# Performance work log

Measured on AMD Instinct MI355X. Metric: run time of the kernel, lower is better.

Reference implementation:

```python
import jax, jax.numpy as jnp
import numpy as np

EPS = 1e-5  # torch InstanceNorm2d default eps


def conv1x1(x, w, b):
    # x: [B,C,H,W], w: [O,C], b: [O]
    return jnp.einsum('bchw,oc->bohw', x, w) + b[None, :, None, None]


def conv3x3(x, w, b):
    y = jax.lax.conv_general_dilated(x, w, (1, 1), 'SAME',
                                     dimension_numbers=('NCHW', 'OIHW', 'NCHW'))
    return y + b[None, :, None, None]


def inorm(x):
    # InstanceNorm2d, affine=False, biased variance
    m = jnp.mean(x, axis=(2, 3), keepdims=True)
    v = jnp.var(x, axis=(2, 3), keepdims=True)
    return (x - m) * jax.lax.rsqrt(v + EPS)


def self_attn(x, wq, bq, wk, bk, wv, bv, gamma):
    B, C, H, W = x.shape
    N = H * W
    q = conv1x1(x, wq, bq).reshape(B, -1, N)   # [B,C/8,N]
    k = conv1x1(x, wk, bk).reshape(B, -1, N)   # [B,C/8,N]
    A = jax.nn.softmax(jnp.einsum('bdn,bdm->bnm', q, k), axis=-1)  # [B,N,N]
    v = conv1x1(x, wv, bv).reshape(B, C, N)    # [B,C,N]
    out = jnp.einsum('bcm,bnm->bcn', v, A).reshape(B, C, H, W)
    return gamma * out + x


def setup_inputs() -> dict:
    key = jax.random.key(0)
    B, C, H, W = 2, 256, 64, 64
    C8 = C // 8
    ks = iter(jax.random.split(key, 40))

    def n(shape, scale=0.05):
        return jax.random.normal(next(ks), shape, dtype=jnp.float32) * scale

    inp = {
        'x': jax.random.normal(next(ks), (B, C, H, W), dtype=jnp.float32),
        'y': jax.random.normal(next(ks), (B, C, H, W), dtype=jnp.float32),
    }
    for p in ('sa1', 'sa2', 'top'):
        inp[p + '_wq'] = n((C8, C)); inp[p + '_bq'] = n((C8,))
        inp[p + '_wk'] = n((C8, C)); inp[p + '_bk'] = n((C8,))
        inp[p + '_wv'] = n((C, C));  inp[p + '_bv'] = n((C,))
        inp[p + '_gamma'] = n((1,), 0.1)
    inp['conv1_w'] = n((C, C, 3, 3)); inp['conv1_b'] = n((C,))
    inp['conv2_w'] = n((C, C, 3, 3)); inp['conv2_b'] = n((C,))
    return inp


def reference(x, y,
              sa1_wq, sa1_bq, sa1_wk, sa1_bk, sa1_wv, sa1_bv, sa1_gamma,
              sa2_wq, sa2_bq, sa2_wk, sa2_bk, sa2_wv, sa2_bv, sa2_gamma,
              top_wq, top_bq, top_wk, top_bk, top_wv, top_bv, top_gamma,
              conv1_w, conv1_b, conv2_w, conv2_b):
    out_1 = inorm(self_attn(x, sa1_wq, sa1_bq, sa1_wk, sa1_bk, sa1_wv, sa1_bv, sa1_gamma))
    out_2 = inorm(out_1 + conv3x3(out_1, conv1_w, conv1_b))
    out_3 = inorm(self_attn(y, sa2_wq, sa2_bq, sa2_wk, sa2_bk, sa2_wv, sa2_bv, sa2_gamma))

    B, C, H, W = out_2.shape
    N = H * W
    q = conv1x1(out_2, top_wq, top_bq).reshape(B, -1, N)
    k = conv1x1(out_2, top_wk, top_bk).reshape(B, -1, N)
    A = jax.nn.softmax(jnp.einsum('bdn,bdm->bnm', q, k), axis=-1)
    v = conv1x1(out_3, top_wv, top_bv).reshape(B, C, N)
    out = jnp.einsum('bcm,bnm->bcn', v, A).reshape(B, C, H, W)
    out = top_gamma * out + y
    out = inorm(out)
    out = inorm(out + out_3)
    out_4 = conv3x3(out, conv2_w, conv2_b)
    out = inorm(out + out_4)
    return out
```

## Files before the change

kernel.cpp:

```cpp
#include <hip/hip_runtime.h>
#include <hip/hip_bf16.h>

typedef __hip_bfloat16 bf16;
typedef __attribute__((ext_vector_type(8))) short s8v;
typedef __attribute__((ext_vector_type(4))) short s4v;
typedef __attribute__((ext_vector_type(4))) float f4v;

#define NPIX 4096
#define CDIM 256
#define MN_ELEMS (1 << 20)
#define QKVSTR (320L * NPIX)
#define QKTSTR (64L * NPIX)

#if __has_builtin(__builtin_amdgcn_exp2f)
#define EXP2F(x) __builtin_amdgcn_exp2f(x)
#else
#define EXP2F(x) exp2f(x)
#endif

typedef __attribute__((address_space(1))) const unsigned int g_u32;
typedef __attribute__((address_space(3))) unsigned int l_u32;
__device__ __forceinline__ void glds16(const void* g, void* l) {
  __builtin_amdgcn_global_load_lds((g_u32*)g, (l_u32*)l, 16, 0, 0);
}

__device__ inline s8v ld8(const bf16* p) { return *(const s8v*)p; }
__device__ inline s8v ld8(const float* p) {
  float4 f0 = *(const float4*)p;
  float4 f1 = *(const float4*)(p + 4);
  s8v r; bf16* e = (bf16*)&r;
  e[0] = __float2bfloat16(f0.x); e[1] = __float2bfloat16(f0.y);
  e[2] = __float2bfloat16(f0.z); e[3] = __float2bfloat16(f0.w);
  e[4] = __float2bfloat16(f1.x); e[5] = __float2bfloat16(f1.y);
  e[6] = __float2bfloat16(f1.z); e[7] = __float2bfloat16(f1.w);
  return r;
}

template<int NT>
__global__ __launch_bounds__(256) void fattn_k(
    const bf16* __restrict__ qkt, const bf16* __restrict__ Vg,
    bf16* __restrict__ out)
{
  constexpr int SN = NT / 32;
  __shared__ bf16 k_s[128 * 32];
  __shared__ bf16 v_s[4 * 128 * 32];
  __shared__ bf16 p_s[4 * NT * 32];
  float* sums = (float*)k_s;

  const int tid = threadIdx.x;
  const int z = blockIdx.z;
  const int w = tid >> 6, lane = tid & 63;
  const int l15 = lane & 15, oct = lane >> 4;
  const int wr = w >> 1, wc = w & 1;
  const int n0 = blockIdx.x * NT, c0 = blockIdx.y * 128;
  const bf16* qk = qkt + (long)z * QKTSTR;
  const bf16* Vz = Vg + (long)z * QKVSTR;
  const int srow = lane >> 2, scol = (lane & 3) * 8;

  #pragma unroll
  for (int g = 0; g < NT / 64; ++g)
    glds16(qk + (long)(n0 + g * 64 + (w << 4) + srow) * 64 + scol,
           p_s + g * 2048 + w * 512);
  glds16(qk + (long)((w << 4) + srow) * 64 + 32 + scol, k_s + w * 512);
  glds16(qk + (long)(64 + (w << 4) + srow) * 64 + 32 + scol, k_s + 2048 + w * 512);
  #pragma unroll
  for (int g = 0; g < 8; ++g) {
    const int kk = g & 3, rg = g >> 2;
    glds16(Vz + (long)(c0 + rg * 64 + (w << 4) + srow) * 4096 + kk * 32 + scol,
           v_s + kk * 4096 + rg * 2048 + w * 512);
  }
  __syncthreads();

  s8v qf[SN];
  #pragma unroll
  for (int st = 0; st < SN; ++st)
    qf[st] = *(const s8v*)(p_s + (wr * (NT / 2) + st * 16 + l15) * 32 + oct * 8);
  __syncthreads();

  f4v acc[4][SN];
  #pragma unroll
  for (int i = 0; i < 4; ++i)
    #pragma unroll
    for (int j = 0; j < SN; ++j) acc[i][j] = (f4v){0.f, 0.f, 0.f, 0.f};
  float rs[SN];
  #pragma unroll
  for (int st = 0; st < SN; ++st) rs[st] = 0.f;

  for (int i = 0; i < 32; ++i) {
    s8v kf[4];
    #pragma unroll
    for (int nt = 0; nt < 4; ++nt)
      kf[nt] = *(const s8v*)(k_s + (wc * 64 + nt * 16 + l15) * 32 + oct * 8);
    #pragma unroll
    for (int st = 0; st < SN; ++st) {
      const int n = wr * (NT / 2) + st * 16 + l15;
      const int sw = ((n >> 1) & 3) << 4;
      f4v sa[4];
      __builtin_amdgcn_s_setprio(1);
      #pragma unroll
      for (int nt = 0; nt < 4; ++nt) {
        f4v zz = (f4v){0.f, 0.f, 0.f, 0.f};
        sa[nt] = __builtin_amdgcn_mfma_f32_16x16x32_bf16(kf[nt], qf[st], zz, 0, 0, 0);
      }
      __builtin_amdgcn_s_setprio(0);
      #pragma unroll
      for (int nt = 0; nt < 4; ++nt) {
        const int kk = wc * 2 + (nt >> 1);
        int byte = kk * (NT * 64) + n * 64 + (nt & 1) * 32 + oct * 8;
        byte ^= sw;
        s4v pk; bf16* pe = (bf16*)&pk;
        float rsum = 0.f;
        #pragma unroll
        for (int r = 0; r < 4; ++r) {
          float e = EXP2F(sa[nt][r]);
          rsum += e;
          pe[r] = __float2bfloat16(e);
        }
        rs[st] += rsum;
        *(s4v*)((char*)p_s + byte) = pk;
      }
    }
    __syncthreads();
    #pragma unroll
    for (int kk = 0; kk < 4; ++kk) {
      s8v vf[4], pf[SN];
      #pragma unroll
      for (int st = 0; st < 4; ++st)
        vf[st] = *(const s8v*)(v_s + kk * 4096 + (wr * 64 + st * 16 + l15) * 32 + oct * 8);
      #pragma unroll
      for (int nt = 0; nt < SN; ++nt) {
        const int n = wc * (NT / 2) + nt * 16 + l15;
        int byte = kk * (NT * 64) + n * 64 + oct * 16;
        byte ^= ((n >> 1) & 3) << 4;
        pf[nt] = *(const s8v*)((const char*)p_s + byte);
      }
      __builtin_amdgcn_s_setprio(1);
      #pragma unroll
      for (int st = 0; st < 4; ++st)
        #pragma unroll
        for (int nt = 0; nt < SN; ++nt)
          acc[st][nt] = __builtin_amdgcn_mfma_f32_16x16x32_bf16(vf[st], pf[nt], acc[st][nt], 0, 0, 0);
      __builtin_amdgcn_s_setprio(0);
    }
    __syncthreads();
    if (i < 31) {
      const int m1 = (i + 1) * 128;
      glds16(qk + (long)(m1 + (w << 4) + srow) * 64 + 32 + scol, k_s + w * 512);
      glds16(qk + (long)(m1 + 64 + (w << 4) + srow) * 64 + 32 + scol, k_s + 2048 + w * 512);
      #pragma unroll
      for (int g = 0; g < 8; ++g) {
        const int kk = g & 3, rg = g >> 2;
        glds16(Vz + (long)(c0 + rg * 64 + (w << 4) + srow) * 4096 + m1 + kk * 32 + scol,
               v_s + kk * 4096 + rg * 2048 + w * 512);
      }
      __syncthreads();
    }
  }

  #pragma unroll
  for (int st = 0; st < SN; ++st) {
    rs[st] += __shfl_xor(rs[st], 16);
    rs[st] += __shfl_xor(rs[st], 32);
  }
  if (lane < 16) {
    #pragma unroll
    for (int st = 0; st < SN; ++st)
      sums[wc * NT + wr * (NT / 2) + st * 16 + l15] = rs[st];
  }
  __syncthreads();

  float rinv[SN];
  #pragma unroll
  for (int nt = 0; nt < SN; ++nt) {
    const int n = wc * (NT / 2) + nt * 16 + l15;
    rinv[nt] = 1.f / (sums[n] + sums[NT + n]);
  }
  bf16* op = out + (long)z * ((long)CDIM * NPIX);
  #pragma unroll
  for (int st = 0; st < 4; ++st) {
    const int gc = c0 + wr * 64 + st * 16 + oct * 4;
    #pragma unroll
    for (int nt = 0; nt < SN; ++nt) {
      const int gn = n0 + wc * (NT / 2) + nt * 16 + l15;
      #pragma unroll
      for (int r = 0; r < 4; ++r)
        op[(long)(gc + r) * NPIX + gn] = __float2bfloat16(acc[st][nt][r] * rinv[nt]);
    }
  }
}

__global__ __launch_bounds__(512) void conv_k(
    const bf16* __restrict__ x, const bf16* __restrict__ wcvt,
    const float* __restrict__ bias, bf16* __restrict__ out)
{
  __shared__ bf16 lds[3 * 66 * 66];
  const int tid = threadIdx.x;
  const int h = blockIdx.x;
  const int o0 = blockIdx.y * 128;
  x   += (long)blockIdx.z * CDIM * NPIX;
  out += (long)blockIdx.z * CDIM * NPIX;

  const int w = tid >> 6, lane = tid & 63;
  const int l15 = lane & 15, oct = lane >> 4;

  if (tid < 192) {
    int row = tid >> 6, c = tid & 63;
    lds[(row * 66 + 0) * 66 + c] = __float2bfloat16(0.f);
    lds[(row * 66 + 65) * 66 + c] = __float2bfloat16(0.f);
  }

  f4v acc[4];
  #pragma unroll
  for (int nf = 0; nf < 4; ++nf) acc[nf] = (f4v){0.f, 0.f, 0.f, 0.f};

  const int w2 = tid & 31, chi = tid >> 5;
  const long arow = (long)(o0 + w * 16 + l15) * 2304;

  for (int cg = 0; cg < 4; ++cg) {
    __syncthreads();
    #pragma unroll
    for (int it = 0; it < 12; ++it) {
      int row = it >> 2, cgi = it & 3;
      int c = cgi * 16 + chi;
      int hh = h + row - 1;
      unsigned int pix = 0;
      if ((unsigned)hh < 64u)
        pix = *(const unsigned int*)(x + (long)(cg * 64 + c) * 4096 + hh * 64 + w2 * 2);
      const bf16* pp = (const bf16*)&pix;
      lds[(row * 66 + (w2 * 2 + 1)) * 66 + c] = pp[0];
      lds[(row * 66 + (w2 * 2 + 2)) * 66 + c] = pp[1];
    }
    __syncthreads();

    #pragma unroll
    for (int j = 0; j < 9; ++j) {
      const int dy = j / 3, dx = j % 3;
      #pragma unroll
      for (int kc = 0; kc < 2; ++kc) {
        s8v af = *(const s8v*)(wcvt + arow + j * 256 + cg * 64 + kc * 32 + oct * 8);
        s8v bfv[4];
        #pragma unroll
        for (int nf = 0; nf < 4; ++nf)
          bfv[nf] = *(const s8v*)&lds[(dy * 66 + (nf * 16 + l15 + dx)) * 66 + kc * 32 + oct * 8];
        #pragma unroll
        for (int nf = 0; nf < 4; ++nf)
          acc[nf] = __builtin_amdgcn_mfma_f32_16x16x32_bf16(af, bfv[nf], acc[nf], 0, 0, 0);
      }
    }
  }

  #pragma unroll
  for (int nf = 0; nf < 4; ++nf) {
    const int gn = h * 64 + nf * 16 + l15;
    const int go = o0 + w * 16 + oct * 4;
    #pragma unroll
    for (int r = 0; r < 4; ++r)
      out[(long)(go + r) * NPIX + gn] = __float2bfloat16(acc[nf][r] + bias[go + r]);
  }
}

template<int QKT, typename TBe>
__global__ __launch_bounds__(256) void proj_k(
    const float* __restrict__ A, const float* __restrict__ A2,
    const TBe* __restrict__ B1, const TBe* __restrict__ B2,
    const float* __restrict__ bias, const float* __restrict__ bias2,
    bf16* __restrict__ Cm, bf16* __restrict__ qkt,
    int M, int N, int K, long bbat, long cbat, int nchunk)
{
  __shared__ bf16 a_s[64][40];
  __shared__ bf16 b_s[64][40];
  const int tid = threadIdx.x;
  const int z = blockIdx.z, stage = z >> 1, bat = z & 1;
  const float* Au = stage ? A2 : A;
  const float* biasu = stage ? bias2 : bias;
  const TBe* Bm = (stage ? B2 : B1) + bat * bbat;
  Cm += z * cbat;
  if (QKT) qkt += z * QKTSTR;
  const int m0 = blockIdx.y * 64, n0 = blockIdx.x * 64;
  const int w = tid >> 6, lane = tid & 63;
  const int l15 = lane & 15, oct = lane >> 4;

  f4v acc[4];
  #pragma unroll
  for (int i = 0; i < 4; ++i) acc[i] = (f4v){0.f, 0.f, 0.f, 0.f};

  const int a_i0 = tid >> 2, a_i1 = (tid & 3) * 8;
  const int b_i0 = tid >> 3, b_i1 = (tid & 7) * 8;

  s8v pa, pb;
  auto ldA = [&](int kc, s8v& d) {
    if (m0 + a_i0 < M) d = ld8(Au + (long)(m0 + a_i0) * K + kc * 32 + a_i1);
    else d = (s8v){0,0,0,0,0,0,0,0};
  };
  auto ldB = [&](int kc, s8v& d) {
    d = ld8(Bm + (long)(kc * 32 + b_i0) * N + n0 + b_i1);
  };

  ldA(0, pa); ldB(0, pb);
  for (int kc = 0; kc < nchunk; ++kc) {
    *(s8v*)&a_s[a_i0][a_i1] = pa;
    {
      const bf16* e = (const bf16*)&pb;
      #pragma unroll
      for (int j = 0; j < 8; ++j) b_s[b_i1 + j][b_i0] = e[j];
    }
    __syncthreads();
    if (kc + 1 < nchunk) { ldA(kc + 1, pa); ldB(kc + 1, pb); }
    s8v af = *(const s8v*)&a_s[w * 16 + l15][oct * 8];
    #pragma unroll
    for (int nt = 0; nt < 4; ++nt) {
      s8v bfr = *(const s8v*)&b_s[nt * 16 + l15][oct * 8];
      acc[nt] = __builtin_amdgcn_mfma_f32_16x16x32_bf16(af, bfr, acc[nt], 0, 0, 0);
    }
    __syncthreads();
  }
  const int gm_base = m0 + w * 16 + oct * 4;
  #pragma unroll
  for (int nt = 0; nt < 4; ++nt) {
    const int gn = n0 + nt * 16 + l15;
    #pragma unroll
    for (int r = 0; r < 4; ++r) {
      int gm = gm_base + r;
      if (gm < M) {
        float vv = acc[nt][r] + biasu[gm];
        if (QKT && gm < 64) {
          float vv2 = (gm < 32) ? vv * 1.44269504f : vv;
          qkt[(long)gn * 64 + gm] = __float2bfloat16(vv2);
        } else {
          Cm[(long)gm * N + gn] = __float2bfloat16(vv);
        }
      }
    }
  }
}

__global__ __launch_bounds__(256) void cat_k(
    const float* __restrict__ wq, const float* __restrict__ bq,
    const float* __restrict__ wk, const float* __restrict__ bk,
    const float* __restrict__ wv, const float* __restrict__ bv,
    float* __restrict__ wcat, float* __restrict__ bcat, int M)
{
  int idx = blockIdx.x * 256 + threadIdx.x;
  int total = M << 8;
  if (idx < total) {
    int r = idx >> 8, c = idx & 255;
    float v;
    if (r < 32) v = wq[r * 256 + c];
    else if (r < 64) v = wk[(r - 32) * 256 + c];
    else v = wv[(r - 64) * 256 + c];
    wcat[idx] = v;
  } else if (idx < total + M) {
    int r = idx - total;
    bcat[r] = (r < 32) ? bq[r] : (r < 64) ? bk[r - 32] : bv[r - 64];
  }
}

__global__ __launch_bounds__(256) void cvtw2_k(
    const float* __restrict__ w1, const float* __restrict__ w2,
    bf16* __restrict__ o1, bf16* __restrict__ o2)
{
  const float* in = blockIdx.y ? w2 : w1;
  bf16* out = blockIdx.y ? o2 : o1;
  int idx = blockIdx.x * 256 + threadIdx.x;
  int o = idx / 2304, r = idx % 2304;
  int j = r >> 8, c = r & 255;
  out[idx] = __float2bfloat16(in[(o * 256 + c) * 9 + j]);
}

__device__ inline void ld16(const bf16* p, float* v) {
  s8v r0 = *(const s8v*)p, r1 = *(const s8v*)(p + 8);
  const bf16* e0 = (const bf16*)&r0; const bf16* e1 = (const bf16*)&r1;
  #pragma unroll
  for (int j = 0; j < 8; ++j) { v[j] = __bfloat162float(e0[j]); v[8 + j] = __bfloat162float(e1[j]); }
}
__device__ inline void ld16(const float* p, float* v) {
  #pragma unroll
  for (int q = 0; q < 4; ++q) {
    float4 f = *(const float4*)(p + q * 4);
    v[q * 4 + 0] = f.x; v[q * 4 + 1] = f.y; v[q * 4 + 2] = f.z; v[q * 4 + 3] = f.w;
  }
}
__device__ inline void st16(bf16* p, const float* v) {
  s8v o0, o1v; bf16* f0 = (bf16*)&o0; bf16* f1 = (bf16*)&o1v;
  #pragma unroll
  for (int j = 0; j < 8; ++j) { f0[j] = __float2bfloat16(v[j]); f1[j] = __float2bfloat16(v[8 + j]); }
  *(s8v*)p = o0; *(s8v*)(p + 8) = o1v;
}
__device__ inline void st16(float* p, const float* v) {
  #pragma unroll
  for (int q = 0; q < 4; ++q) {
    float4 f; f.x = v[q * 4 + 0]; f.y = v[q * 4 + 1]; f.z = v[q * 4 + 2]; f.w = v[q * 4 + 3];
    *(float4*)(p + q * 4) = f;
  }
}

template<typename TAe, typename TBe, typename TOe, int G>
__global__ __launch_bounds__(256) void inorm_k(
    const TAe* __restrict__ a, const TBe* __restrict__ b,
    const float* __restrict__ g, TOe* __restrict__ out)
{
  __shared__ float red[8];
  const int tid = threadIdx.x;
  const long base = (long)blockIdx.x * NPIX + tid * 16;
  float gv = G ? *g : 1.f;
  float va[16], vbv[16], v[16];
  ld16(a + base, va);
  ld16(b + base, vbv);
  #pragma unroll
  for (int j = 0; j < 16; ++j) v[j] = gv * va[j] + vbv[j];
  float sum = 0.f, sq = 0.f;
  #pragma unroll
  for (int j = 0; j < 16; ++j) { sum += v[j]; sq += v[j] * v[j]; }
  #pragma unroll
  for (int s = 32; s; s >>= 1) { sum += __shfl_xor(sum, s); sq += __shfl_xor(sq, s); }
  if ((tid & 63) == 0) { red[tid >> 6] = sum; red[4 + (tid >> 6)] = sq; }
  __syncthreads();
  sum = red[0] + red[1] + red[2] + red[3];
  sq  = red[4] + red[5] + red[6] + red[7];
  float mean = sum * (1.f / NPIX);
  float var  = fmaxf(sq * (1.f / NPIX) - mean * mean, 0.f);
  float rstd = rsqrtf(var + 1e-5f);
  float o[16];
  #pragma unroll
  for (int j = 0; j < 16; ++j) o[j] = (v[j] - mean) * rstd;
  st16(out + base, o);
}

static const long CN = (long)CDIM * NPIX;

static void attn_core(int nb, bf16* qkv, bf16* qkt, bf16* t0, hipStream_t stream)
{
  fattn_k<64><<<dim3(64, 2, nb), dim3(256), 0, stream>>>(qkt, qkv + 64 * NPIX, t0);
}

static void run_conv(const bf16* src, const bf16* wcvt, const float* cb,
                     bf16* dst, hipStream_t stream)
{
  conv_k<<<dim3(64, 2, 2), dim3(512), 0, stream>>>(src, wcvt, cb, dst);
}

extern "C" void kernel_launch(void* const* d_in, const int* in_sizes, int n_in,
                              void* d_out, int out_size, void* d_ws, size_t ws_size,
                              hipStream_t stream)
{
  (void)in_sizes; (void)n_in; (void)out_size; (void)ws_size;
  const float* x = (const float*)d_in[0];
  const float* y = (const float*)d_in[1];
  auto W = [&](int i) { return (const float*)d_in[i]; };

  char* wp = (char*)d_ws;
  auto take = [&](size_t nbytes) { char* p = wp; wp += (nbytes + 255) & ~(size_t)255; return p; };
  bf16*  qkv   = (bf16*)take((size_t)4 * QKVSTR * 2);
  bf16*  qkt   = (bf16*)take((size_t)4 * QKTSTR * 2);
  bf16*  t0    = (bf16*)take((size_t)4 * CN * 2);
  bf16*  u1    = (bf16*)take(2 * CN * 2);
  bf16*  u2    = (bf16*)take(2 * CN * 2);
  bf16*  u3    = (bf16*)take(2 * CN * 2);
  bf16*  u4    = (bf16*)take(2 * CN * 2);
  bf16*  wcvt1 = (bf16*)take((size_t)589824 * 2);
  bf16*  wcvt2 = (bf16*)take((size_t)589824 * 2);
  float* wcat1 = (float*)take((size_t)81920 * 4);
  float* bcat1 = (float*)take(320 * 4);
  float* wcat2 = (float*)take((size_t)81920 * 4);
  float* bcat2 = (float*)take(320 * 4);
  float* wqk   = (float*)take((size_t)16384 * 4);
  float* bqk   = (float*)take(64 * 4);
  bf16*  cvout = qkv;

  dim3 TB(256);

  cat_k<<<dim3(322), TB, 0, stream>>>(W(2), W(3), W(4), W(5), W(6), W(7), wcat1, bcat1, 320);
  cat_k<<<dim3(322), TB, 0, stream>>>(W(9), W(10), W(11), W(12), W(13), W(14), wcat2, bcat2, 320);
  cat_k<<<dim3(65),  TB, 0, stream>>>(W(16), W(17), W(18), W(19), nullptr, nullptr, wqk, bqk, 64);
  cvtw2_k<<<dim3(2304, 2), TB, 0, stream>>>(W(23), W(25), wcvt1, wcvt2);

  proj_k<1,float><<<dim3(64,5,4), TB, 0, stream>>>(
      wcat1, wcat2, x, y, bcat1, bcat2, qkv, qkt, 320, NPIX, 256, CN, QKVSTR, 8);
  attn_core(4, qkv, qkt, t0, stream);

  inorm_k<bf16,float,bf16,1><<<dim3(512), TB, 0, stream>>>(t0, x, W(8), u1);
  inorm_k<bf16,float,bf16,1><<<dim3(512), TB, 0, stream>>>(t0 + 2 * CN, y, W(15), u3);

  run_conv(u1, wcvt1, W(24), cvout, stream);
  inorm_k<bf16,bf16,bf16,0><<<dim3(512), TB, 0, stream>>>(u1, cvout, nullptr, u2);

  proj_k<1,bf16><<<dim3(64,1,2), TB, 0, stream>>>(
      wqk, wqk, u2, u2, bqk, bqk, qkv, qkt, 64, NPIX, 256, CN, QKVSTR, 8);
  proj_k<0,bf16><<<dim3(64,4,2), TB, 0, stream>>>(
      W(20), W(20), u3, u3, W(21), W(21), qkv + 64 * NPIX, qkt, 256, NPIX, 256, CN, QKVSTR, 8);
  attn_core(2, qkv, qkt, t0, stream);
  inorm_k<bf16,float,bf16,1><<<dim3(512), TB, 0, stream>>>(t0, y, W(22), u1);
  inorm_k<bf16,bf16,bf16,0><<<dim3(512), TB, 0, stream>>>(u1, u3, nullptr, u4);
  run_conv(u4, wcvt2, W(26), cvout, stream);
  inorm_k<bf16,bf16,float,0><<<dim3(512), TB, 0, stream>>>(u4, cvout, nullptr, (float*)d_out);
}
```

Baseline: 381.4 us.

## Split fused attention block across eight waves instead of four

The flash-attention kernel now runs 512 threads (8 waves) per block, with the same 64-query by 128-channel tile. Each wave computes a smaller 32x32 slice of the score matrix and of the P·V accumulation, and the row sums are reduced across four column groups. The goal is more waves in flight to hide LDS and MFMA latency and to spread the cooperative global-to-LDS loads. The cost is more barrier participants and less register-level reuse per wave.

```diff
diff --git a/kernel.cpp b/kernel.cpp
--- a/kernel.cpp
+++ b/kernel.cpp
@@ -36,77 +36,67 @@
   return r;
 }
 
-template<int NT>
-__global__ __launch_bounds__(256) void fattn_k(
+__global__ __launch_bounds__(512) void fattn_k(
     const bf16* __restrict__ qkt, const bf16* __restrict__ Vg,
     bf16* __restrict__ out)
 {
-  constexpr int SN = NT / 32;
   __shared__ bf16 k_s[128 * 32];
   __shared__ bf16 v_s[4 * 128 * 32];
-  __shared__ bf16 p_s[4 * NT * 32];
+  __shared__ bf16 p_s[4 * 64 * 32];
   float* sums = (float*)k_s;
 
   const int tid = threadIdx.x;
   const int z = blockIdx.z;
   const int w = tid >> 6, lane = tid & 63;
   const int l15 = lane & 15, oct = lane >> 4;
-  const int wr = w >> 1, wc = w & 1;
-  const int n0 = blockIdx.x * NT, c0 = blockIdx.y * 128;
+  const int wr2 = w >> 2, wc2 = w & 3;
+  const int pc = w >> 1, pn = w & 1;
+  const int n0 = blockIdx.x * 64, c0 = blockIdx.y * 128;
   const bf16* qk = qkt + (long)z * QKTSTR;
   const bf16* Vz = Vg + (long)z * QKVSTR;
-  const int srow = lane >> 2, scol = (lane & 3) * 8;
-
-  #pragma unroll
-  for (int g = 0; g < NT / 64; ++g)
-    glds16(qk + (long)(n0 + g * 64 + (w << 4) + srow) * 64 + scol,
-           p_s + g * 2048 + w * 512);
-  glds16(qk + (long)((w << 4) + srow) * 64 + 32 + scol, k_s + w * 512);
-  glds16(qk + (long)(64 + (w << 4) + srow) * 64 + 32 + scol, k_s + 2048 + w * 512);
-  #pragma unroll
-  for (int g = 0; g < 8; ++g) {
-    const int kk = g & 3, rg = g >> 2;
-    glds16(Vz + (long)(c0 + rg * 64 + (w << 4) + srow) * 4096 + kk * 32 + scol,
-           v_s + kk * 4096 + rg * 2048 + w * 512);
-  }
+  const int t2 = tid >> 2, t3 = (tid & 3) * 8;
+
+  if (tid < 256)
+    glds16(qk + (long)(n0 + t2) * 64 + t3, p_s + tid * 8);
+  glds16(qk + (long)t2 * 64 + 32 + t3, k_s + tid * 8);
+  #pragma unroll
+  for (int g = 0; g < 4; ++g)
+    glds16(Vz + (long)(c0 + t2) * 4096 + g * 32 + t3, v_s + g * 4096 + tid * 8);
   __syncthreads();
 
-  s8v qf[SN];
-  #pragma unroll
-  for (int st = 0; st < SN; ++st)
-    qf[st] = *(const s8v*)(p_s + (wr * (NT / 2) + st * 16 + l15) * 32 + oct * 8);
+  s8v qf[2];
+  #pragma unroll
+  for (int st = 0; st < 2; ++st)
+    qf[st] = *(const s8v*)(p_s + (wr2 * 32 + st * 16 + l15) * 32 + oct * 8);
   __syncthreads();
 
-  f4v acc[4][SN];
-  #pragma unroll
-  for (int i = 0; i < 4; ++i)
-    #pragma unroll
-    for (int j = 0; j < SN; ++j) acc[i][j] = (f4v){0.f, 0.f, 0.f, 0.f};
-  float rs[SN];
-  #pragma unroll
-  for (int st = 0; st < SN; ++st) rs[st] = 0.f;
+  f4v acc[2][2];
+  #pragma unroll
+  for (int i = 0; i < 2; ++i)
+    #pragma unroll
+    for (int j = 0; j < 2; ++j) acc[i][j] = (f4v){0.f, 0.f, 0.f, 0.f};
+  float rs[2] = {0.f, 0.f};
 
   for (int i = 0; i < 32; ++i) {
-    s8v kf[4];
-    #pragma unroll
-    for (int nt = 0; nt < 4; ++nt)
-      kf[nt] = *(const s8v*)(k_s + (wc * 64 + nt * 16 + l15) * 32 + oct * 8);
-    #pragma unroll
-    for (int st = 0; st < SN; ++st) {
-      const int n = wr * (NT / 2) + st * 16 + l15;
+    s8v kf[2];
+    #pragma unroll
+    for (int nt = 0; nt < 2; ++nt)
+      kf[nt] = *(const s8v*)(k_s + (wc2 * 32 + nt * 16 + l15) * 32 + oct * 8);
+    #pragma unroll
+    for (int st = 0; st < 2; ++st) {
+      const int n = wr2 * 32 + st * 16 + l15;
       const int sw = ((n >> 1) & 3) << 4;
-      f4v sa[4];
+      f4v sa[2];
       __builtin_amdgcn_s_setprio(1);
       #pragma unroll
-      for (int nt = 0; nt < 4; ++nt) {
+      for (int nt = 0; nt < 2; ++nt) {
         f4v zz = (f4v){0.f, 0.f, 0.f, 0.f};
         sa[nt] = __builtin_amdgcn_mfma_f32_16x16x32_bf16(kf[nt], qf[st], zz, 0, 0, 0);
       }
       __builtin_amdgcn_s_setprio(0);
       #pragma unroll
-      for (int nt = 0; nt < 4; ++nt) {
-        const int kk = wc * 2 + (nt >> 1);
-        int byte = kk * (NT * 64) + n * 64 + (nt & 1) * 32 + oct * 8;
+      for (int nt = 0; nt < 2; ++nt) {
+        int byte = wc2 * 4096 + n * 64 + nt * 32 + oct * 8;
         byte ^= sw;
         s4v pk; bf16* pe = (bf16*)&pk;
         float rsum = 0.f;
@@ -123,65 +113,61 @@
     __syncthreads();
     #pragma unroll
     for (int kk = 0; kk < 4; ++kk) {
-      s8v vf[4], pf[SN];
-      #pragma unroll
-      for (int st = 0; st < 4; ++st)
-        vf[st] = *(const s8v*)(v_s + kk * 4096 + (wr * 64 + st * 16 + l15) * 32 + oct * 8);
-      #pragma unroll
-      for (int nt = 0; nt < SN; ++nt) {
-        const int n = wc * (NT / 2) + nt * 16 + l15;
-        int byte = kk * (NT * 64) + n * 64 + oct * 16;
+      s8v vf[2], pf[2];
+      #pragma unroll
+      for (int st = 0; st < 2; ++st)
+        vf[st] = *(const s8v*)(v_s + kk * 4096 + (pc * 32 + st * 16 + l15) * 32 + oct * 8);
+      #pragma unroll
+      for (int nt = 0; nt < 2; ++nt) {
+        const int n = pn * 32 + nt * 16 + l15;
+        int byte = kk * 4096 + n * 64 + oct * 16;
         byte ^= ((n >> 1) & 3) << 4;
         pf[nt] = *(const s8v*)((const char*)p_s + byte);
       }
       __builtin_amdgcn_s_setprio(1);
       #pragma unroll
-      for (int st = 0; st < 4; ++st)
+      for (int st = 0; st < 2; ++st)
         #pragma unroll
-        for (int nt = 0; nt < SN; ++nt)
+        for (int nt = 0; nt < 2; ++nt)
           acc[st][nt] = __builtin_amdgcn_mfma_f32_16x16x32_bf16(vf[st], pf[nt], acc[st][nt], 0, 0, 0);
       __builtin_amdgcn_s_setprio(0);
     }
     __syncthreads();
     if (i < 31) {
       const int m1 = (i + 1) * 128;
-      glds16(qk + (long)(m1 + (w << 4) + srow) * 64 + 32 + scol, k_s + w * 512);
-      glds16(qk + (long)(m1 + 64 + (w << 4) + srow) * 64 + 32 + scol, k_s + 2048 + w * 512);
-      #pragma unroll
-      for (int g = 0; g < 8; ++g) {
-        const int kk = g & 3, rg = g >> 2;
-        glds16(Vz + (long)(c0 + rg * 64 + (w << 4) + srow) * 4096 + m1 + kk * 32 + scol,
-               v_s + kk * 4096 + rg * 2048 + w * 512);
-      }
+      glds16(qk + (long)(m1 + t2) * 64 + 32 + t3, k_s + tid * 8);
+      #pragma unroll
+      for (int g = 0; g < 4; ++g)
+        glds16(Vz + (long)(c0 + t2) * 4096 + m1 + g * 32 + t3, v_s + g * 4096 + tid * 8);
       __syncthreads();
     }
   }
 
   #pragma unroll
-  for (int st = 0; st < SN; ++st) {
+  for (int st = 0; st < 2; ++st) {
     rs[st] += __shfl_xor(rs[st], 16);
     rs[st] += __shfl_xor(rs[st], 32);
   }
   if (lane < 16) {
     #pragma unroll
-    for (int st = 0; st < SN; ++st)
-      sums[wc * NT + wr * (NT / 2) + st * 16 + l15] = rs[st];
+    for (int st = 0; st < 2; ++st)
+      sums[wc2 * 64 + wr2 * 32 + st * 16 + l15] = rs[st];
   }
   __syncthreads();
 
-  float rinv[SN];
-  #pragma unroll
-  for (int nt = 0; nt < SN; ++nt) {
-    const int n = wc * (NT / 2) + nt * 16 + l15;
-    rinv[nt] = 1.f / (sums[n] + sums[NT + n]);
+  float rinv[2];
+  #pragma unroll
+  for (int nt = 0; nt < 2; ++nt) {
+    const int n = pn * 32 + nt * 16 + l15;
+    rinv[nt] = 1.f / (sums[n] + sums[64 + n] + sums[128 + n] + sums[192 + n]);
   }
   bf16* op = out + (long)z * ((long)CDIM * NPIX);
   #pragma unroll
-  for (int st = 0; st < 4; ++st) {
-    const int gc = c0 + wr * 64 + st * 16 + oct * 4;
-    #pragma unroll
-    for (int nt = 0; nt < SN; ++nt) {
-      const int gn = n0 + wc * (NT / 2) + nt * 16 + l15;
+  for (int st = 0; st < 2; ++st) {
+    const int gc = c0 + pc * 32 + st * 16 + oct * 4;
+    #pragma unroll
+    for (int nt = 0; nt < 2; ++nt) {
+      const int gn = n0 + pn * 32 + nt * 16 + l15;
       #pragma unroll
       for (int r = 0; r < 4; ++r)
         op[(long)(gc + r) * NPIX + gn] = __float2bfloat16(acc[st][nt][r] * rinv[nt]);
@@ -430,7 +416,7 @@
 
 static void attn_core(int nb, bf16* qkv, bf16* qkt, bf16* t0, hipStream_t stream)
 {
-  fattn_k<64><<<dim3(64, 2, nb), dim3(256), 0, stream>>>(qkt, qkv + 64 * NPIX, t0);
+  fattn_k<<<dim3(64, 2, nb), dim3(512), 0, stream>>>(qkt, qkv + 64 * NPIX, t0);
 }
 
 static void run_conv(const bf16* src, const bf16* wcvt, const float* cb,
```

Result: faster. 366.7 us (-3.9%).
